# Performance work log

Measured on AMD Instinct MI355X. Metric: run time of the kernel, lower is better.

## Reference

```python
import math
import jax, jax.numpy as jnp
import numpy as np

B, T, C = 2, 2048, 1024
N_HEAD = 16
HEAD_DIM = C // N_HEAD

def setup_inputs() -> dict:
    key = jax.random.key(0)
    kx, kq, kk, kv, kp = jax.random.split(key, 5)
    s = 1.0 / math.sqrt(C)
    return {
        "x": jax.random.normal(kx, (B, T, C), dtype=jnp.float32),
        "Wq": jax.random.normal(kq, (C, C), dtype=jnp.float32) * s,
        "Wk": jax.random.normal(kk, (C, C), dtype=jnp.float32) * s,
        "Wv": jax.random.normal(kv, (C, C), dtype=jnp.float32) * s,
        "Wproj": jax.random.normal(kp, (C, C), dtype=jnp.float32) * s,
    }

def reference(x, Wq, Wk, Wv, Wproj):
    b, t, c = x.shape
    # nn.Linear(no bias): x @ W.T ; weights stored [out, in]
    def heads(w):
        return (x @ w.T).reshape(b, t, N_HEAD, HEAD_DIM).transpose(0, 2, 1, 3)  # [B,H,T,D]
    q, k, v = heads(Wq), heads(Wk), heads(Wv)
    att = jnp.einsum('bhqd,bhkd->bhqk', q, k) / math.sqrt(HEAD_DIM)  # [B,H,T,T]
    causal = jnp.tril(jnp.ones((t, t), dtype=bool))
    att = jnp.where(causal, att, -jnp.inf)
    att = jax.nn.softmax(att, axis=-1)
    y = jnp.einsum('bhqk,bhkd->bhqd', att, v)           # [B,H,T,D]
    y = y.transpose(0, 2, 1, 3).reshape(b, t, c)        # [B,T,C]
    return y @ Wproj.T
```

## Files before the change

### kernel.cpp

```cpp
#include <hip/hip_runtime.h>
#include <stdint.h>

typedef uint16_t u16;
typedef uint32_t u32;
typedef __attribute__((ext_vector_type(8))) _Float16 f16x8;
typedef __attribute__((ext_vector_type(4))) float f32x4;

#define NB 2
#define NT 2048
#define NC 1024
#define NH 16
#define ND 64
#define NM (NB*NT)
#define LOG2E 1.44269504088896340736f

__device__ __forceinline__ u16 f2h(float f) {
  _Float16 h = (_Float16)f;
  return __builtin_bit_cast(u16, h);
}

__global__ __launch_bounds__(256) void cvt_kernel(const float* __restrict__ src,
                                                  u16* __restrict__ dst, int n4) {
  int i = blockIdx.x * 256 + threadIdx.x;
  if (i >= n4) return;
  float4 v = ((const float4*)src)[i];
  ushort4 o;
  o.x = f2h(v.x); o.y = f2h(v.y); o.z = f2h(v.z); o.w = f2h(v.w);
  ((ushort4*)dst)[i] = o;
}

__global__ __launch_bounds__(256) void cvtw_kernel(const float* __restrict__ w0,
                                                   const float* __restrict__ w1,
                                                   const float* __restrict__ w2,
                                                   const float* __restrict__ w3,
                                                   u16* __restrict__ dst) {
  int i = blockIdx.x * 256 + threadIdx.x;
  int which = i >> 18;
  const float* src = (which == 0) ? w0 : (which == 1) ? w1 : (which == 2) ? w2 : w3;
  int j = i & 262143;
  float4 v = ((const float4*)src)[j];
  ushort4 o;
  o.x = f2h(v.x); o.y = f2h(v.y); o.z = f2h(v.z); o.w = f2h(v.w);
  ((ushort4*)dst)[i] = o;
}

__device__ __forceinline__ void gload16(const void* g, void* l) {
  __builtin_amdgcn_global_load_lds(
      (const __attribute__((address_space(1))) void*)g,
      (__attribute__((address_space(3))) void*)l, 16, 0, 0);
}

template<int EPI>
__global__ __launch_bounds__(256) void gemm_bt(const u16* __restrict__ A,
                                               const u16* __restrict__ Bw,
                                               int K, int N,
                                               u16* __restrict__ oq, u16* __restrict__ okk,
                                               u16* __restrict__ ovt,
                                               float* __restrict__ of) {
  __shared__ __align__(16) u16 SH[2*128*64];
  u16* Al = SH;
  u16* Bl = SH + 128*64;
  const int tid = threadIdx.x, lane = tid & 63, wid = tid >> 6;
  const int g = lane >> 4, qq = lane & 15;
  const int wm = wid >> 1, wn = wid & 1;
  const int m0 = blockIdx.y * 128, n0 = blockIdx.x * 128;
  const int srow = lane >> 3;
  const int scol = (lane & 7) * 8;

  f32x4 acc[4][4] = {};

  for (int kt = 0; kt < K; kt += 64) {
    #pragma unroll
    for (int pp = 0; pp < 4; ++pp) {
      int r = wid*32 + pp*8;
      gload16(A  + (size_t)(m0 + r + srow)*K + kt + scol, &Al[r*64]);
      gload16(Bw + (size_t)(n0 + r + srow)*K + kt + scol, &Bl[r*64]);
    }
    __syncthreads();
    #pragma unroll
    for (int kk = 0; kk < 2; ++kk) {
      f16x8 af[4], bfr[4];
      #pragma unroll
      for (int mt = 0; mt < 4; ++mt)
        af[mt] = *(const f16x8*)&Al[(wm*64 + mt*16 + qq)*64 + kk*32 + 8*g];
      #pragma unroll
      for (int nt = 0; nt < 4; ++nt)
        bfr[nt] = *(const f16x8*)&Bl[(wn*64 + nt*16 + qq)*64 + kk*32 + 8*g];
      #pragma unroll
      for (int mt = 0; mt < 4; ++mt)
        #pragma unroll
        for (int nt = 0; nt < 4; ++nt)
          acc[mt][nt] = __builtin_amdgcn_mfma_f32_16x16x32_f16(af[mt], bfr[nt], acc[mt][nt], 0, 0, 0);
    }
    __syncthreads();
  }

  if (EPI == 0) {
    u16* reg = SH + wid*4096;
    const int sel = n0 >> 10;
    const int h = ((n0 & 1023) >> 6) + wn;
    const int bq = m0 >> 11;

    if (sel < 2) {
      const float scale = (sel == 0) ? 0.125f*LOG2E : 1.0f;
      #pragma unroll
      for (int mt = 0; mt < 4; ++mt)
        #pragma unroll
        for (int r = 0; r < 4; ++r) {
          int mloc = mt*16 + g*4 + r;
          #pragma unroll
          for (int nt = 0; nt < 4; ++nt) {
            int d = nt*16 + qq;
            reg[mloc*64 + (d ^ (g << 4))] = f2h(acc[mt][nt][r] * scale);
          }
        }
      u16* dst = (sel == 0) ? oq : okk;
      const int slot = lane & 7;
      #pragma unroll
      for (int i = 0; i < 8; ++i) {
        int row = i*8 + (lane >> 3);
        int physslot = slot ^ (((row >> 2) & 3) << 1);
        f16x8 vvv = *(const f16x8*)&reg[row*64 + physslot*8];
        int m = m0 + wm*64 + row;
        int t = m & (NT-1);
        *(f16x8*)(dst + (((size_t)(bq*NH + h)*NT + t)*ND) + slot*8) = vvv;
      }
    } else {
      #pragma unroll
      for (int nt = 0; nt < 4; ++nt) {
        int d = nt*16 + qq;
        int f = (d & 7) << 3;
        #pragma unroll
        for (int mt = 0; mt < 4; ++mt)
          #pragma unroll
          for (int rp = 0; rp < 2; ++rp) {
            int r = rp*2;
            int mloc = mt*16 + g*4 + r;
            u32 pk = (u32)f2h(acc[mt][nt][r]) | ((u32)f2h(acc[mt][nt][r+1]) << 16);
            *(u32*)&reg[d*64 + (mloc ^ f)] = pk;
          }
      }
      const int slot = lane & 7;
      const int t0 = m0 + wm*64;
      #pragma unroll
      for (int i = 0; i < 8; ++i) {
        int d = i*8 + (lane >> 3);
        int physslot = slot ^ (d & 7);
        f16x8 vvv = *(const f16x8*)&reg[d*64 + physslot*8];
        int t = (t0 & (NT-1)) + slot*8;
        *(f16x8*)(ovt + ((size_t)(bq*NH + h)*ND + d)*NT + t) = vvv;
      }
    }
  } else {
    #pragma unroll
    for (int mt = 0; mt < 4; ++mt)
      #pragma unroll
      for (int r = 0; r < 4; ++r) {
        int m = m0 + wm*64 + mt*16 + g*4 + r;
        #pragma unroll
        for (int nt = 0; nt < 4; ++nt) {
          int n = n0 + wn*64 + nt*16 + qq;
          of[(size_t)m*N + n] = acc[mt][nt][r];
        }
      }
  }
}

__global__ __launch_bounds__(256) void attn_kernel(const u16* __restrict__ q,
                                                   const u16* __restrict__ k,
                                                   const u16* __restrict__ vt,
                                                   u16* __restrict__ y) {
  __shared__ __align__(16) u16 Kl[2][64*64];
  __shared__ __align__(16) u16 Vl[2][64*64];
  __shared__ __align__(16) u16 Pl[4*16*64];
  const int tid = threadIdx.x, lane = tid & 63, wid = tid >> 6;
  const int g = lane >> 4, qq = lane & 15;
  const int bh = blockIdx.x;
  const int yy = blockIdx.y;
  const int hmap4[4] = {0, 31, 8, 23};
  const int qtile = yy ^ hmap4[yy >> 3];
  const int qs = qtile * 64;
  const u16* qp = q  + (size_t)bh*NT*ND;
  const u16* kp = k  + (size_t)bh*NT*ND;
  const u16* vp = vt + (size_t)bh*ND*NT;
  const int b = bh >> 4, h = bh & 15;
  const int srow = lane >> 3;
  const int scol8 = (lane & 7) ^ (srow & 7);
  u16* pl = &Pl[wid*1024];
  u32* plw = (u32*)pl;

  f16x8 aq[2];
  {
    int t = qs + wid*16 + qq;
    #pragma unroll
    for (int c = 0; c < 2; ++c)
      aq[c] = *(const f16x8*)(qp + (size_t)t*ND + c*32 + 8*g);
  }

  f16x8 vones;
  #pragma unroll
  for (int i = 0; i < 8; ++i) vones[i] = (_Float16)1.0f;

  f32x4 accO[4] = {};
  f32x4 accS = {};
  float m_run = -1e30f;

  const int ntiles = qtile + 1;

  #pragma unroll
  for (int pp = 0; pp < 2; ++pp) {
    int issue = wid*2 + pp;
    int row = issue*8 + srow;
    gload16(kp + (size_t)row*ND + scol8*8, &Kl[0][issue*512]);
    gload16(vp + (size_t)row*NT + scol8*8, &Vl[0][issue*512]);
  }

  for (int kt = 0; kt < ntiles; ++kt) {
    const int kvs = kt*64;
    const int cur = kt & 1;
    __syncthreads();

    if (kt + 1 < ntiles) {
      const int kvs2 = kvs + 64;
      #pragma unroll
      for (int pp = 0; pp < 2; ++pp) {
        int issue = wid*2 + pp;
        int row = issue*8 + srow;
        gload16(kp + (size_t)(kvs2 + row)*ND + scol8*8, &Kl[cur^1][issue*512]);
        gload16(vp + (size_t)row*NT + kvs2 + scol8*8, &Vl[cur^1][issue*512]);
      }
    }

    f32x4 sacc[4] = {};
    __builtin_amdgcn_s_setprio(1);
    #pragma unroll
    for (int c = 0; c < 2; ++c) {
      #pragma unroll
      for (int nt = 0; nt < 4; ++nt) {
        int row = nt*16 + qq;
        int col = (c*32 + 8*g) ^ ((row & 7) << 3);
        f16x8 kb = *(const f16x8*)&Kl[cur][row*64 + col];
        sacc[nt] = __builtin_amdgcn_mfma_f32_16x16x32_f16(kb, aq[c], sacc[nt], 0, 0, 0);
      }
    }
    __builtin_amdgcn_s_setprio(0);

    if (kvs + 63 > qs + wid*16) {
      int qg = qs + wid*16 + qq;
      #pragma unroll
      for (int nt = 0; nt < 4; ++nt)
        #pragma unroll
        for (int r = 0; r < 4; ++r)
          if (kvs + nt*16 + g*4 + r > qg) sacc[nt][r] = -1e30f;
    }

    float m0a = fmaxf(fmaxf(sacc[0][0], sacc[0][1]), fmaxf(sacc[0][2], sacc[0][3]));
    float m1a = fmaxf(fmaxf(sacc[1][0], sacc[1][1]), fmaxf(sacc[1][2], sacc[1][3]));
    float m2a = fmaxf(fmaxf(sacc[2][0], sacc[2][1]), fmaxf(sacc[2][2], sacc[2][3]));
    float m3a = fmaxf(fmaxf(sacc[3][0], sacc[3][1]), fmaxf(sacc[3][2], sacc[3][3]));
    float mloc = fmaxf(fmaxf(m0a, m1a), fmaxf(m2a, m3a));

    const bool defer = __all(mloc <= m_run + 8.f);
    float mnew;
    if (defer) {
      mnew = m_run;
    } else {
      float mf = fmaxf(mloc, __shfl_xor(mloc, 16));
      mf = fmaxf(mf, __shfl_xor(mf, 32));
      mnew = fmaxf(m_run, mf);
      float a = exp2f(m_run - mnew);
      m_run = mnew;
      #pragma unroll
      for (int r = 0; r < 4; ++r) {
        float ar = __shfl(a, (lane & 48) + g*4 + r);
        #pragma unroll
        for (int nt = 0; nt < 4; ++nt) accO[nt][r] *= ar;
        accS[r] *= ar;
      }
    }

    #pragma unroll
    for (int nt = 0; nt < 4; ++nt) {
      float p0 = exp2f(sacc[nt][0] - mnew);
      float p1 = exp2f(sacc[nt][1] - mnew);
      float p2 = exp2f(sacc[nt][2] - mnew);
      float p3 = exp2f(sacc[nt][3] - mnew);
      u32 pk0 = __builtin_bit_cast(u32, __builtin_amdgcn_cvt_pkrtz(p0, p1));
      u32 pk1 = __builtin_bit_cast(u32, __builtin_amdgcn_cvt_pkrtz(p2, p3));
      int kv0 = nt*16 + g*4;
      plw[(qq*64 + (kv0 ^ ((qq & 7) << 3))) >> 1] = pk0;
      plw[(qq*64 + ((kv0 + 2) ^ ((qq & 7) << 3))) >> 1] = pk1;
    }

    __builtin_amdgcn_s_setprio(1);
    #pragma unroll
    for (int c = 0; c < 2; ++c) {
      f16x8 pa = *(const f16x8*)&pl[qq*64 + ((c*32 + 8*g) ^ ((qq & 7) << 3))];
      accS = __builtin_amdgcn_mfma_f32_16x16x32_f16(pa, vones, accS, 0, 0, 0);
      #pragma unroll
      for (int nt = 0; nt < 4; ++nt) {
        int vrow = nt*16 + qq;
        int vcol = (c*32 + 8*g) ^ ((vrow & 7) << 3);
        f16x8 vb = *(const f16x8*)&Vl[cur][vrow*64 + vcol];
        accO[nt] = __builtin_amdgcn_mfma_f32_16x16x32_f16(pa, vb, accO[nt], 0, 0, 0);
      }
    }
    __builtin_amdgcn_s_setprio(0);
  }

  #pragma unroll
  for (int r = 0; r < 4; ++r) {
    float invr = 1.0f / accS[r];
    int t = qs + wid*16 + g*4 + r;
    #pragma unroll
    for (int nt = 0; nt < 4; ++nt) {
      int d = nt*16 + qq;
      y[((size_t)(b*NT + t))*NC + h*ND + d] = f2h(accO[nt][r] * invr);
    }
  }
}

extern "C" void kernel_launch(void* const* d_in, const int* in_sizes, int n_in,
                              void* d_out, int out_size, void* d_ws, size_t ws_size,
                              hipStream_t stream) {
  const float* x  = (const float*)d_in[0];
  const float* Wq = (const float*)d_in[1];
  const float* Wk = (const float*)d_in[2];
  const float* Wv = (const float*)d_in[3];
  const float* Wp = (const float*)d_in[4];

  u16* xb   = (u16*)d_ws;
  u16* wqkv = xb   + (size_t)NM*NC;
  u16* wpj  = wqkv + (size_t)3*NC*NC;
  u16* qb   = wpj  + (size_t)NC*NC;
  u16* kb   = qb   + (size_t)NM*NC;
  u16* vtb  = kb   + (size_t)NM*NC;
  u16* yb   = vtb  + (size_t)NM*NC;
  size_t need = ((size_t)NM*NC*5 + (size_t)4*NC*NC) * sizeof(u16);
  if (ws_size < need) return;

  cvt_kernel<<<NM*NC/4/256, 256, 0, stream>>>(x, xb, NM*NC/4);
  cvtw_kernel<<<4*NC*NC/4/256, 256, 0, stream>>>(Wq, Wk, Wv, Wp, wqkv);

  gemm_bt<0><<<dim3(3*NC/128, NM/128), 256, 0, stream>>>(xb, wqkv, NC, 3*NC,
                                                         qb, kb, vtb, nullptr);
  attn_kernel<<<dim3(NB*NH, 32), 256, 0, stream>>>(qb, kb, vtb, yb);
  gemm_bt<1><<<dim3(NC/128, NM/128), 256, 0, stream>>>(yb, wpj, NC, NC,
                                                       nullptr, nullptr, nullptr,
                                                       (float*)d_out);
}
```

Before: 134.6 us.

## Double-buffer GEMM LDS tiles and XOR-swizzle columns to avoid bank conflicts

Doubles the GEMM shared-memory buffer so the next K-tile's global-to-LDS loads are issued while the current tile feeds the MFMAs, with a single barrier per iteration. It also XOR-swizzles the 16-byte column chunks by row when loading and reading, to reduce LDS bank conflicts on the fragment reads. LDS use grows to 64KB per block, which may lower occupancy.

```diff
diff --git a/kernel.cpp b/kernel.cpp
--- a/kernel.cpp
+++ b/kernel.cpp
@@ -57,45 +57,61 @@
                                                u16* __restrict__ oq, u16* __restrict__ okk,
                                                u16* __restrict__ ovt,
                                                float* __restrict__ of) {
-  __shared__ __align__(16) u16 SH[2*128*64];
+  __shared__ __align__(16) u16 SH[4*128*64];
   u16* Al = SH;
-  u16* Bl = SH + 128*64;
+  u16* Bl = SH + 2*128*64;
   const int tid = threadIdx.x, lane = tid & 63, wid = tid >> 6;
   const int g = lane >> 4, qq = lane & 15;
   const int wm = wid >> 1, wn = wid & 1;
   const int m0 = blockIdx.y * 128, n0 = blockIdx.x * 128;
   const int srow = lane >> 3;
-  const int scol = (lane & 7) * 8;
+  const int scol8 = (lane & 7) ^ srow;
 
   f32x4 acc[4][4] = {};
-
-  for (int kt = 0; kt < K; kt += 64) {
-    #pragma unroll
-    for (int pp = 0; pp < 4; ++pp) {
-      int r = wid*32 + pp*8;
-      gload16(A  + (size_t)(m0 + r + srow)*K + kt + scol, &Al[r*64]);
-      gload16(Bw + (size_t)(n0 + r + srow)*K + kt + scol, &Bl[r*64]);
-    }
+  const int nk = K >> 6;
+
+  #pragma unroll
+  for (int pp = 0; pp < 4; ++pp) {
+    int r = wid*32 + pp*8;
+    gload16(A  + (size_t)(m0 + r + srow)*K + scol8*8, &Al[r*64]);
+    gload16(Bw + (size_t)(n0 + r + srow)*K + scol8*8, &Bl[r*64]);
+  }
+
+  for (int kt = 0; kt < nk; ++kt) {
+    const int cur = kt & 1;
     __syncthreads();
+    if (kt + 1 < nk) {
+      const int k1 = (kt + 1) << 6;
+      #pragma unroll
+      for (int pp = 0; pp < 4; ++pp) {
+        int r = wid*32 + pp*8;
+        gload16(A  + (size_t)(m0 + r + srow)*K + k1 + scol8*8, &Al[(cur^1)*8192 + r*64]);
+        gload16(Bw + (size_t)(n0 + r + srow)*K + k1 + scol8*8, &Bl[(cur^1)*8192 + r*64]);
+      }
+    }
     #pragma unroll
     for (int kk = 0; kk < 2; ++kk) {
       f16x8 af[4], bfr[4];
       #pragma unroll
-      for (int mt = 0; mt < 4; ++mt)
-        af[mt] = *(const f16x8*)&Al[(wm*64 + mt*16 + qq)*64 + kk*32 + 8*g];
-      #pragma unroll
-      for (int nt = 0; nt < 4; ++nt)
-        bfr[nt] = *(const f16x8*)&Bl[(wn*64 + nt*16 + qq)*64 + kk*32 + 8*g];
+      for (int mt = 0; mt < 4; ++mt) {
+        int row = wm*64 + mt*16 + qq;
+        af[mt] = *(const f16x8*)&Al[cur*8192 + row*64 + (((kk*4 + g) ^ (qq & 7))*8)];
+      }
+      #pragma unroll
+      for (int nt = 0; nt < 4; ++nt) {
+        int row = wn*64 + nt*16 + qq;
+        bfr[nt] = *(const f16x8*)&Bl[cur*8192 + row*64 + (((kk*4 + g) ^ (qq & 7))*8)];
+      }
       #pragma unroll
       for (int mt = 0; mt < 4; ++mt)
         #pragma unroll
         for (int nt = 0; nt < 4; ++nt)
           acc[mt][nt] = __builtin_amdgcn_mfma_f32_16x16x32_f16(af[mt], bfr[nt], acc[mt][nt], 0, 0, 0);
     }
+  }
+
+  if (EPI == 0) {
     __syncthreads();
-  }
-
-  if (EPI == 0) {
     u16* reg = SH + wid*4096;
     const int sel = n0 >> 10;
     const int h = ((n0 & 1023) >> 6) + wn;
```

Result: faster. 115.8 us (-13.9%).
